# Optimization experiments

Hardware: AMD Instinct MI355X
Metric: run time of the kernel (lower is better)

Reference implementation:

```python
import jax, jax.numpy as jnp
import numpy as np

D = 2048
HQ = 16
HKV = 4
HEAD_DIM = D // HQ  # 128
REP = HQ // HKV     # 4


def setup_inputs() -> dict:
    key = jax.random.key(0)
    kx, kq, kk, kv, ko = jax.random.split(key, 5)
    B, S = 2, 2048
    scale = 1.0 / np.sqrt(D)
    return {
        "x": jax.random.normal(kx, (B, S, D), dtype=jnp.float32),
        "Wq": jax.random.normal(kq, (D, HQ * HEAD_DIM), dtype=jnp.float32) * scale,
        "Wk": jax.random.normal(kk, (D, HKV * HEAD_DIM), dtype=jnp.float32) * scale,
        "Wv": jax.random.normal(kv, (D, HKV * HEAD_DIM), dtype=jnp.float32) * scale,
        "Wo": jax.random.normal(ko, (D, D), dtype=jnp.float32) * scale,
    }


def reference(x, Wq, Wk, Wv, Wo):
    B, S, _ = x.shape
    # projections
    q = (x @ Wq).reshape(B, S, HQ, HEAD_DIM).transpose(0, 2, 1, 3)    # [B,Hq,S,d]
    k = (x @ Wk).reshape(B, S, HKV, HEAD_DIM).transpose(0, 2, 1, 3)   # [B,Hkv,S,d]
    v = (x @ Wv).reshape(B, S, HKV, HEAD_DIM).transpose(0, 2, 1, 3)
    # GQA: repeat_interleave KV heads to match query heads
    k = jnp.repeat(k, REP, axis=1)  # [B,Hq,S,d]
    v = jnp.repeat(v, REP, axis=1)
    scores = jnp.einsum("bhqd,bhkd->bhqk", q, k) / jnp.sqrt(
        jnp.asarray(HEAD_DIM, dtype=x.dtype))
    attn = jax.nn.softmax(scores, axis=-1)
    out = jnp.einsum("bhqk,bhkd->bhqd", attn, v)          # [B,Hq,S,d]
    out = out.transpose(0, 2, 1, 3).reshape(B, S, HQ * HEAD_DIM)
    return out @ Wo
```

## Files before the change

### kernel.cpp

```cpp
#include <hip/hip_runtime.h>
#include <stdint.h>

typedef __bf16 bf16;
typedef __attribute__((ext_vector_type(4))) float f32x4;
typedef __attribute__((ext_vector_type(16))) float f32x16;
typedef __attribute__((ext_vector_type(8))) bf16 bf16x8;
typedef __attribute__((ext_vector_type(4))) bf16 bf16x4;
typedef __attribute__((ext_vector_type(4))) float f4;

#define HQ_ 16
#define HKV_ 4
#define S_ 2048
#define D_ 2048

static __device__ __forceinline__ void gload16(const void* g, void* lds_base) {
  __builtin_amdgcn_global_load_lds(
      (const __attribute__((address_space(1))) void*)g,
      (__attribute__((address_space(3))) void*)lds_base, 16, 0, 0);
}

static __device__ __forceinline__ uint32_t pk2(float a, float b) {
  uint16_t lo = __builtin_bit_cast(uint16_t, (bf16)a);
  uint16_t hi = __builtin_bit_cast(uint16_t, (bf16)b);
  return (uint32_t)lo | ((uint32_t)hi << 16);
}

__global__ __launch_bounds__(256) void cast_x(const float* __restrict__ in,
                                              bf16* __restrict__ out, int n4) {
  int i = blockIdx.x * 256 + threadIdx.x;
  if (i >= n4) return;
  f4 v = *(const f4*)(in + (size_t)i * 4);
  bf16x4 o;
  o[0] = (bf16)v[0]; o[1] = (bf16)v[1]; o[2] = (bf16)v[2]; o[3] = (bf16)v[3];
  *(bf16x4*)(out + (size_t)i * 4) = o;
}

__global__ __launch_bounds__(256) void transW(const float* __restrict__ W,
                                              bf16* __restrict__ Wt, int K, int N,
                                              float scale) {
  __shared__ float tile[32][33];
  int n0 = blockIdx.x * 32, k0 = blockIdx.y * 32;
  int tx = threadIdx.x & 31, ty = threadIdx.x >> 5;
#pragma unroll
  for (int i = 0; i < 4; ++i)
    tile[ty + i * 8][tx] = W[(size_t)(k0 + ty + i * 8) * N + n0 + tx];
  __syncthreads();
#pragma unroll
  for (int i = 0; i < 4; ++i)
    Wt[(size_t)(n0 + ty + i * 8) * K + k0 + tx] = (bf16)(tile[tx][ty + i * 8] * scale);
}

template <int MODE>
__global__ __launch_bounds__(256, 3)
void gemm128(const bf16* __restrict__ A, const bf16* __restrict__ Bt,
             void* __restrict__ out, void* __restrict__ out2,
             void* __restrict__ out3, int K, int N) {
  __shared__ __align__(16) bf16 As[2][128 * 32];
  __shared__ __align__(16) bf16 Bs[2][128 * 32];
  const int t = threadIdx.x;
  const int lane = t & 63, wave = t >> 6;
  const int l16 = lane & 15, l4 = lane >> 4;
  const int wr = wave >> 1, wc = wave & 1;
  const int m0 = blockIdx.y * 128, n0 = blockIdx.x * 128;

  f32x4 acc[4][4] = {};

  const int r0 = t >> 2, c0 = ((t & 3) ^ ((t >> 3) & 3));
  const int r1 = r0 + 64, c1 = ((t & 3) ^ ((r1 >> 1) & 3));
  const bf16* aS0 = A + (size_t)(m0 + r0) * K + c0 * 8;
  const bf16* aS1 = A + (size_t)(m0 + r1) * K + c1 * 8;
  const bf16* bS0 = Bt + (size_t)(n0 + r0) * K + c0 * 8;
  const bf16* bS1 = Bt + (size_t)(n0 + r1) * K + c1 * 8;

  const int nk = K >> 5;
  auto STAGE = [&](int buf, int kt) {
    gload16(aS0 + (size_t)kt * 32, &As[buf][(wave * 64) * 8]);
    gload16(aS1 + (size_t)kt * 32, &As[buf][(256 + wave * 64) * 8]);
    gload16(bS0 + (size_t)kt * 32, &Bs[buf][(wave * 64) * 8]);
    gload16(bS1 + (size_t)kt * 32, &Bs[buf][(256 + wave * 64) * 8]);
  };

  STAGE(0, 0);
  int cb = 0;
  for (int kt = 0; kt < nk; ++kt) {
    int kn = kt + 1; if (kn == nk) kn = 0;
    STAGE(cb ^ 1, kn);
    asm volatile("s_waitcnt vmcnt(4)" ::: "memory");
    __builtin_amdgcn_s_barrier();
    bf16x8 af[4], bb[4];
#pragma unroll
    for (int mf = 0; mf < 4; ++mf) {
      int row = wr * 64 + mf * 16 + l16;
      af[mf] = *(const bf16x8*)&As[cb][row * 32 + (l4 ^ ((row >> 1) & 3)) * 8];
    }
#pragma unroll
    for (int nf = 0; nf < 4; ++nf) {
      int row = wc * 64 + nf * 16 + l16;
      bb[nf] = *(const bf16x8*)&Bs[cb][row * 32 + (l4 ^ ((row >> 1) & 3)) * 8];
    }
#pragma unroll
    for (int mf = 0; mf < 4; ++mf)
#pragma unroll
      for (int nf = 0; nf < 4; ++nf)
        acc[mf][nf] = __builtin_amdgcn_mfma_f32_16x16x32_bf16(af[mf], bb[nf],
                                                              acc[mf][nf], 0, 0, 0);
    __builtin_amdgcn_s_barrier();
    cb ^= 1;
  }

#pragma unroll
  for (int mf = 0; mf < 4; ++mf)
#pragma unroll
    for (int nf = 0; nf < 4; ++nf)
#pragma unroll
      for (int rg = 0; rg < 4; ++rg) {
        int r = m0 + wr * 64 + mf * 16 + l4 * 4 + rg;
        int c = n0 + wc * 64 + nf * 16 + l16;
        float v = acc[mf][nf][rg];
        if constexpr (MODE == 4) {
          int b = r >> 11, s = r & 2047;
          if (c < 2048) {
            int h = c >> 7, dd = c & 127;
            ((bf16*)out)[(((size_t)(b * HQ_ + h)) * S_ + s) * 128 + dd] = (bf16)v;
          } else if (c < 2560) {
            int cc = c - 2048, h = cc >> 7, dd = cc & 127;
            ((bf16*)out2)[(((size_t)(b * HKV_ + h)) * S_ + s) * 128 + dd] = (bf16)v;
          } else {
            int cc = c - 2560, h = cc >> 7, dd = cc & 127;
            ((bf16*)out3)[(((size_t)(b * HKV_ + h)) * 128 + dd) * S_ + s] = (bf16)v;
          }
        } else {
          ((float*)out)[(size_t)r * N + c] = v;
        }
      }
}

__global__ __launch_bounds__(256, 2)
void attn_fwd(const bf16* __restrict__ Qb, const bf16* __restrict__ Kb,
              const bf16* __restrict__ Vtb, bf16* __restrict__ AO) {
  __shared__ __align__(16) bf16 KS[3][64 * 128];
  __shared__ __align__(16) bf16 VS[2][128 * 64];

  const int flat = blockIdx.x + (blockIdx.y << 4) + (blockIdx.z << 8);
  const int lid = (flat & 7) * 64 + (flat >> 3);
  const int qt = lid & 15, h = (lid >> 4) & 15, b = lid >> 8;
  const int hkv = h >> 2;
  const int t = threadIdx.x, lane = t & 63, wave = t >> 6;
  const int l31 = lane & 31, l32 = lane >> 5;
  const bf16* Qg = Qb + ((size_t)(b * HQ_ + h) * S_ + qt * 128) * 128;
  const bf16* Kg = Kb + (size_t)(b * HKV_ + hkv) * S_ * 128;
  const bf16* Vg = Vtb + (size_t)(b * HKV_ + hkv) * 128 * S_;

  bf16x8 qfr[8];
#pragma unroll
  for (int ds = 0; ds < 8; ++ds)
    qfr[ds] = *(const bf16x8*)&Qg[(size_t)(wave * 32 + l31) * 128 + ds * 16 + l32 * 8];
  asm volatile("s_waitcnt vmcnt(0)" ::: "memory");

  const bf16* kp[4]; const bf16* vp[4];
#pragma unroll
  for (int i = 0; i < 4; ++i) {
    int s = i * 256 + t;
    int kr = s >> 4, klc = (s & 15) ^ (kr & 15);
    kp[i] = Kg + (size_t)kr * 128 + klc * 8;
    int vr = s >> 3, vlc = (s & 7) ^ (vr & 7);
    vp[i] = Vg + (size_t)vr * S_ + vlc * 8;
  }
  auto STAGE_K = [&](int buf, int nt) {
#pragma unroll
    for (int i = 0; i < 4; ++i)
      gload16(kp[i] + (size_t)nt * 8192, &KS[buf][(i * 256 + wave * 64) * 8]);
  };
  auto STAGE_V = [&](int buf, int nt) {
#pragma unroll
    for (int i = 0; i < 4; ++i)
      gload16(vp[i] + nt * 64, &VS[buf][(i * 256 + wave * 64) * 8]);
  };

  f32x16 ao[4] = {};
  float lrun = 0.f;

  STAGE_K(0, 0); STAGE_V(0, 0); STAGE_K(1, 1);
  asm volatile("s_waitcnt vmcnt(8)" ::: "memory");

  int ck = 0, cs = 2, cv = 0;
  for (int nt = 0; nt < S_ / 64; ++nt) {
    STAGE_K(cs, (nt + 2) & 31);
    __builtin_amdgcn_s_barrier();

    f32x16 scT[2] = {};
    __builtin_amdgcn_s_setprio(1);
#pragma unroll
    for (int ds = 0; ds < 8; ++ds) {
      int lc = ds * 2 + l32;
      bf16x8 kb0 = *(const bf16x8*)&KS[ck][l31 * 128 + (lc ^ (l31 & 15)) * 8];
      bf16x8 kb1 = *(const bf16x8*)&KS[ck][(32 + l31) * 128 + (lc ^ (l31 & 15)) * 8];
      scT[0] = __builtin_amdgcn_mfma_f32_32x32x16_bf16(kb0, qfr[ds], scT[0], 0, 0, 0);
      scT[1] = __builtin_amdgcn_mfma_f32_32x32x16_bf16(kb1, qfr[ds], scT[1], 0, 0, 0);
    }
    __builtin_amdgcn_s_setprio(0);

    float ssum = 0.f;
#pragma unroll
    for (int kf = 0; kf < 2; ++kf)
#pragma unroll
      for (int r = 0; r < 16; ++r) {
        float pv = __builtin_amdgcn_exp2f(scT[kf][r]);
        scT[kf][r] = pv;
        ssum += pv;
      }
    lrun += ssum;

    uint32_t u[2][4][2];
#pragma unroll
    for (int kf = 0; kf < 2; ++kf)
#pragma unroll
      for (int g = 0; g < 4; ++g)
#pragma unroll
        for (int j = 0; j < 2; ++j)
          u[kf][g][j] = pk2(scT[kf][g * 4 + 2 * j], scT[kf][g * 4 + 2 * j + 1]);

    bf16x8 pb[4];
#pragma unroll
    for (int ks = 0; ks < 4; ++ks) {
      int kf = ks >> 1, bb = ks & 1;
      uint32_t d0 = u[kf][2 * bb][0], s0 = u[kf][2 * bb + 1][0];
      uint32_t d1 = u[kf][2 * bb][1], s1 = u[kf][2 * bb + 1][1];
      asm volatile("v_permlane32_swap_b32 %0, %1" : "+v"(d0), "+v"(s0));
      asm volatile("v_permlane32_swap_b32 %0, %1" : "+v"(d1), "+v"(s1));
      uint4 w; w.x = d0; w.y = d1; w.z = s0; w.w = s1;
      pb[ks] = __builtin_bit_cast(bf16x8, w);
    }

    asm volatile("s_waitcnt vmcnt(4)" ::: "memory");
    __builtin_amdgcn_s_barrier();
    STAGE_V(cv ^ 1, (nt + 1) & 31);

    __builtin_amdgcn_s_setprio(1);
#pragma unroll
    for (int ks = 0; ks < 4; ++ks) {
      int lc = ks * 2 + l32;
#pragma unroll
      for (int df = 0; df < 4; ++df) {
        int dd = df * 32 + l31;
        bf16x8 va = *(const bf16x8*)&VS[cv][dd * 64 + (lc ^ (l31 & 7)) * 8];
        ao[df] = __builtin_amdgcn_mfma_f32_32x32x16_bf16(va, pb[ks], ao[df], 0, 0, 0);
      }
    }
    __builtin_amdgcn_s_setprio(0);

    ck = (ck == 2) ? 0 : ck + 1;
    cs = (cs == 2) ? 0 : cs + 1;
    cv ^= 1;
  }

  lrun += __shfl_xor(lrun, 32);
  float inv = 1.f / lrun;
  bf16* aop = AO + ((size_t)(b * S_ + qt * 128 + wave * 32 + l31)) * D_ + h * 128;
#pragma unroll
  for (int df = 0; df < 4; ++df)
#pragma unroll
    for (int g = 0; g < 4; ++g) {
      bf16x4 o;
#pragma unroll
      for (int j = 0; j < 4; ++j) o[j] = (bf16)(ao[df][4 * g + j] * inv);
      *(bf16x4*)&aop[df * 32 + 8 * g + 4 * l32] = o;
    }
}

extern "C" void kernel_launch(void* const* d_in, const int* in_sizes, int n_in,
                              void* d_out, int out_size, void* d_ws, size_t ws_size,
                              hipStream_t stream) {
  const float* x  = (const float*)d_in[0];
  const float* Wq = (const float*)d_in[1];
  const float* Wk = (const float*)d_in[2];
  const float* Wv = (const float*)d_in[3];
  const float* Wo = (const float*)d_in[4];

  char* ws = (char*)d_ws;
  bf16* xb  = (bf16*)(ws + 0);
  bf16* Wqt = (bf16*)(ws + 16777216);
  bf16* Wkt = (bf16*)(ws + 25165824);
  bf16* Wvt = (bf16*)(ws + 27262976);
  bf16* Wot = (bf16*)(ws + 29360128);
  bf16* Qb  = (bf16*)(ws + 37748736);
  bf16* Kb  = (bf16*)(ws + 54525952);
  bf16* Vtb = (bf16*)(ws + 58720256);
  bf16* AO  = xb;

  const float CQ = 1.4426950408889634f * 0.08838834764831845f;

  cast_x<<<8192, 256, 0, stream>>>(x, xb, 2097152);
  transW<<<dim3(64, 64), 256, 0, stream>>>(Wq, Wqt, 2048, 2048, CQ);
  transW<<<dim3(16, 64), 256, 0, stream>>>(Wk, Wkt, 2048, 512, 1.0f);
  transW<<<dim3(16, 64), 256, 0, stream>>>(Wv, Wvt, 2048, 512, 1.0f);
  transW<<<dim3(64, 64), 256, 0, stream>>>(Wo, Wot, 2048, 2048, 1.0f);

  gemm128<4><<<dim3(24, 32), 256, 0, stream>>>(xb, Wqt, (void*)Qb, (void*)Kb,
                                               (void*)Vtb, 2048, 3072);

  attn_fwd<<<dim3(16, 16, 2), 256, 0, stream>>>(Qb, Kb, Vtb, AO);

  gemm128<3><<<dim3(16, 32), 256, 0, stream>>>(AO, Wot, d_out, nullptr, nullptr,
                                               2048, 2048);
}
```

Before: 223.0 us.

## Halve attention KV tile to 32 rows for higher occupancy; swizzle GEMM block order

The attention kernel now processes 32 keys per iteration instead of 64, which halves the K/V shared-memory buffers and the score registers, and raises the launch bound to 4 blocks per CU. The V LDS layout and its XOR swizzle are changed to match the narrower tile. Separately, the GEMM kernel remaps block indices in groups of 8 so that neighbouring blocks are spread across the grid, intended to improve L2 locality or balance across XCDs. In exchange there are twice as many loop iterations and barriers per key sweep, and less MFMA work is available to hide latency within each one.

```diff
diff --git a/kernel.cpp b/kernel.cpp
--- a/kernel.cpp
+++ b/kernel.cpp
@@ -61,7 +61,12 @@
   const int lane = t & 63, wave = t >> 6;
   const int l16 = lane & 15, l4 = lane >> 4;
   const int wr = wave >> 1, wc = wave & 1;
-  const int m0 = blockIdx.y * 128, n0 = blockIdx.x * 128;
+
+  const int gx = gridDim.x;
+  const int flat = blockIdx.x + blockIdx.y * gx;
+  const int chunk = (gx * gridDim.y) >> 3;
+  const int lid = (flat & 7) * chunk + (flat >> 3);
+  const int m0 = (lid / gx) * 128, n0 = (lid % gx) * 128;
 
   f32x4 acc[4][4] = {};
 
@@ -135,11 +140,11 @@
       }
 }
 
-__global__ __launch_bounds__(256, 2)
+__global__ __launch_bounds__(256, 4)
 void attn_fwd(const bf16* __restrict__ Qb, const bf16* __restrict__ Kb,
               const bf16* __restrict__ Vtb, bf16* __restrict__ AO) {
-  __shared__ __align__(16) bf16 KS[3][64 * 128];
-  __shared__ __align__(16) bf16 VS[2][128 * 64];
+  __shared__ __align__(16) bf16 KS[3][32 * 128];
+  __shared__ __align__(16) bf16 VS[2][128 * 32];
 
   const int flat = blockIdx.x + (blockIdx.y << 4) + (blockIdx.z << 8);
   const int lid = (flat & 7) * 64 + (flat >> 3);
@@ -157,94 +162,87 @@
     qfr[ds] = *(const bf16x8*)&Qg[(size_t)(wave * 32 + l31) * 128 + ds * 16 + l32 * 8];
   asm volatile("s_waitcnt vmcnt(0)" ::: "memory");
 
-  const bf16* kp[4]; const bf16* vp[4];
-#pragma unroll
-  for (int i = 0; i < 4; ++i) {
+  const bf16* kp[2]; const bf16* vp[2];
+#pragma unroll
+  for (int i = 0; i < 2; ++i) {
     int s = i * 256 + t;
     int kr = s >> 4, klc = (s & 15) ^ (kr & 15);
     kp[i] = Kg + (size_t)kr * 128 + klc * 8;
-    int vr = s >> 3, vlc = (s & 7) ^ (vr & 7);
+    int vr = s >> 2, vlc = (s & 3) ^ ((vr >> 1) & 3);
     vp[i] = Vg + (size_t)vr * S_ + vlc * 8;
   }
   auto STAGE_K = [&](int buf, int nt) {
 #pragma unroll
-    for (int i = 0; i < 4; ++i)
-      gload16(kp[i] + (size_t)nt * 8192, &KS[buf][(i * 256 + wave * 64) * 8]);
+    for (int i = 0; i < 2; ++i)
+      gload16(kp[i] + (size_t)nt * 4096, &KS[buf][(i * 256 + wave * 64) * 8]);
   };
   auto STAGE_V = [&](int buf, int nt) {
 #pragma unroll
-    for (int i = 0; i < 4; ++i)
-      gload16(vp[i] + nt * 64, &VS[buf][(i * 256 + wave * 64) * 8]);
+    for (int i = 0; i < 2; ++i)
+      gload16(vp[i] + nt * 32, &VS[buf][(i * 256 + wave * 64) * 8]);
   };
 
   f32x16 ao[4] = {};
   float lrun = 0.f;
 
   STAGE_K(0, 0); STAGE_V(0, 0); STAGE_K(1, 1);
-  asm volatile("s_waitcnt vmcnt(8)" ::: "memory");
+  asm volatile("s_waitcnt vmcnt(4)" ::: "memory");
 
   int ck = 0, cs = 2, cv = 0;
-  for (int nt = 0; nt < S_ / 64; ++nt) {
-    STAGE_K(cs, (nt + 2) & 31);
+  for (int nt = 0; nt < S_ / 32; ++nt) {
+    STAGE_K(cs, (nt + 2) & 63);
     __builtin_amdgcn_s_barrier();
 
-    f32x16 scT[2] = {};
+    f32x16 scT = {};
     __builtin_amdgcn_s_setprio(1);
 #pragma unroll
     for (int ds = 0; ds < 8; ++ds) {
       int lc = ds * 2 + l32;
-      bf16x8 kb0 = *(const bf16x8*)&KS[ck][l31 * 128 + (lc ^ (l31 & 15)) * 8];
-      bf16x8 kb1 = *(const bf16x8*)&KS[ck][(32 + l31) * 128 + (lc ^ (l31 & 15)) * 8];
-      scT[0] = __builtin_amdgcn_mfma_f32_32x32x16_bf16(kb0, qfr[ds], scT[0], 0, 0, 0);
-      scT[1] = __builtin_amdgcn_mfma_f32_32x32x16_bf16(kb1, qfr[ds], scT[1], 0, 0, 0);
+      bf16x8 kb = *(const bf16x8*)&KS[ck][l31 * 128 + (lc ^ (l31 & 15)) * 8];
+      scT = __builtin_amdgcn_mfma_f32_32x32x16_bf16(kb, qfr[ds], scT, 0, 0, 0);
     }
     __builtin_amdgcn_s_setprio(0);
 
     float ssum = 0.f;
 #pragma unroll
-    for (int kf = 0; kf < 2; ++kf)
-#pragma unroll
-      for (int r = 0; r < 16; ++r) {
-        float pv = __builtin_amdgcn_exp2f(scT[kf][r]);
-        scT[kf][r] = pv;
-        ssum += pv;
-      }
+    for (int r = 0; r < 16; ++r) {
+      float pv = __builtin_amdgcn_exp2f(scT[r]);
+      scT[r] = pv;
+      ssum += pv;
+    }
     lrun += ssum;
 
-    uint32_t u[2][4][2];
-#pragma unroll
-    for (int kf = 0; kf < 2; ++kf)
-#pragma unroll
-      for (int g = 0; g < 4; ++g)
-#pragma unroll
-        for (int j = 0; j < 2; ++j)
-          u[kf][g][j] = pk2(scT[kf][g * 4 + 2 * j], scT[kf][g * 4 + 2 * j + 1]);
-
-    bf16x8 pb[4];
-#pragma unroll
-    for (int ks = 0; ks < 4; ++ks) {
-      int kf = ks >> 1, bb = ks & 1;
-      uint32_t d0 = u[kf][2 * bb][0], s0 = u[kf][2 * bb + 1][0];
-      uint32_t d1 = u[kf][2 * bb][1], s1 = u[kf][2 * bb + 1][1];
+    uint32_t u[4][2];
+#pragma unroll
+    for (int g = 0; g < 4; ++g)
+#pragma unroll
+      for (int j = 0; j < 2; ++j)
+        u[g][j] = pk2(scT[g * 4 + 2 * j], scT[g * 4 + 2 * j + 1]);
+
+    bf16x8 pb[2];
+#pragma unroll
+    for (int bb = 0; bb < 2; ++bb) {
+      uint32_t d0 = u[2 * bb][0], s0 = u[2 * bb + 1][0];
+      uint32_t d1 = u[2 * bb][1], s1 = u[2 * bb + 1][1];
       asm volatile("v_permlane32_swap_b32 %0, %1" : "+v"(d0), "+v"(s0));
       asm volatile("v_permlane32_swap_b32 %0, %1" : "+v"(d1), "+v"(s1));
       uint4 w; w.x = d0; w.y = d1; w.z = s0; w.w = s1;
-      pb[ks] = __builtin_bit_cast(bf16x8, w);
-    }
-
-    asm volatile("s_waitcnt vmcnt(4)" ::: "memory");
+      pb[bb] = __builtin_bit_cast(bf16x8, w);
+    }
+
+    asm volatile("s_waitcnt vmcnt(2)" ::: "memory");
     __builtin_amdgcn_s_barrier();
-    STAGE_V(cv ^ 1, (nt + 1) & 31);
+    STAGE_V(cv ^ 1, (nt + 1) & 63);
 
     __builtin_amdgcn_s_setprio(1);
 #pragma unroll
-    for (int ks = 0; ks < 4; ++ks) {
-      int lc = ks * 2 + l32;
+    for (int bb = 0; bb < 2; ++bb) {
+      int lc = bb * 2 + l32;
 #pragma unroll
       for (int df = 0; df < 4; ++df) {
         int dd = df * 32 + l31;
-        bf16x8 va = *(const bf16x8*)&VS[cv][dd * 64 + (lc ^ (l31 & 7)) * 8];
-        ao[df] = __builtin_amdgcn_mfma_f32_32x32x16_bf16(va, pb[ks], ao[df], 0, 0, 0);
+        bf16x8 va = *(const bf16x8*)&VS[cv][dd * 32 + (lc ^ ((dd >> 1) & 3)) * 8];
+        ao[df] = __builtin_amdgcn_mfma_f32_32x32x16_bf16(va, pb[bb], ao[df], 0, 0, 0);
       }
     }
     __builtin_amdgcn_s_setprio(0);
```

New measurement: 279.0 us. 25.1% more time.
